# Kernel tuning notes

Measured on AMD Instinct MI355X. Metric: run time of the kernel, lower is better.

The kernel has to match this reference:

```python
import jax, jax.numpy as jnp
import numpy as np

EMBED = 1024
HEADS = 16
HEAD_DIM = EMBED // HEADS


def setup_inputs() -> dict:
    key = jax.random.key(0)
    ks = jax.random.split(key, 12)
    B, S, E = 2, 2048, EMBED
    scale = 1.0 / np.sqrt(E)
    inp = {
        "query": jax.random.normal(ks[0], (B, S, E), jnp.float32),
        "key": jax.random.normal(ks[1], (B, S, E), jnp.float32),
        "value": jax.random.normal(ks[2], (B, S, E), jnp.float32),
        "Wq": jax.random.normal(ks[3], (E, E), jnp.float32) * scale,
        "bq": jax.random.normal(ks[4], (E,), jnp.float32) * 0.01,
        "Wk": jax.random.normal(ks[5], (E, E), jnp.float32) * scale,
        "bk": jax.random.normal(ks[6], (E,), jnp.float32) * 0.01,
        "Wv": jax.random.normal(ks[7], (E, E), jnp.float32) * scale,
        "bv": jax.random.normal(ks[8], (E,), jnp.float32) * 0.01,
        "Wo": jax.random.normal(ks[9], (E, E), jnp.float32) * scale,
        "bo": jax.random.normal(ks[10], (E,), jnp.float32) * 0.01,
    }
    return inp


def reference(query, key, value, Wq, bq, Wk, bk, Wv, bv, Wo, bo):
    B, Sq, E = query.shape
    Sk = key.shape[1]
    H, D = HEADS, HEAD_DIM
    # QKV projections (torch Linear: x @ W.T + b)
    q = (query @ Wq.T + bq).reshape(B, Sq, H, D)
    k = (key @ Wk.T + bk).reshape(B, Sk, H, D)
    v = (value @ Wv.T + bv).reshape(B, Sk, H, D)
    # energy: [B, H, Sq, Sk]; note scale = 1/sqrt(embed_size), not head_dim
    energy = jnp.einsum("bqhd,bkhd->bhqk", q, k)
    scale = jnp.asarray(E, energy.dtype) ** 0.5
    attn = jax.nn.softmax(energy / scale, axis=-1)
    out = jnp.einsum("bhqk,bkhd->bqhd", attn, v).reshape(B, Sq, E)
    # fc_out (dropout is identity at eval)
    return out @ Wo.T + bo
```

## Files before the change

### kernel.cpp

```cpp
#include <hip/hip_runtime.h>
#include <hip/hip_bf16.h>

typedef __hip_bfloat16 bf16;
typedef short frag8 __attribute__((ext_vector_type(8)));
typedef _Float16 half4 __attribute__((ext_vector_type(4)));
typedef _Float16 half8 __attribute__((ext_vector_type(8)));
typedef __fp16 fp16x2 __attribute__((ext_vector_type(2)));
typedef float f32x4 __attribute__((ext_vector_type(4)));

typedef __attribute__((address_space(3))) void lds_void;
typedef __attribute__((address_space(1))) const void gbl_void;

__device__ __forceinline__ void gld16(const void* g, void* l) {
  __builtin_amdgcn_global_load_lds((gbl_void*)g, (lds_void*)l, 16, 0, 0);
}

__device__ __forceinline__ unsigned short f2bf(float f) {
  union { float f; unsigned u; } x; x.f = f;
  unsigned r = x.u + 0x7FFFu + ((x.u >> 16) & 1u);
  return (unsigned short)(r >> 16);
}

#define QSCALE 0.0450842200278f
#define MFIX 4.0f

struct CvtArgs {
  const float4* src[7];
  ushort4* dst[7];
  int n4[7];
};
__global__ __launch_bounds__(256) void cvt_all(CvtArgs a) {
  const int t = blockIdx.y;
  const int i = blockIdx.x * 256 + threadIdx.x;
  if (i >= a.n4[t]) return;
  float4 v = a.src[t][i];
  ushort4 o;
  o.x = f2bf(v.x); o.y = f2bf(v.y); o.z = f2bf(v.z); o.w = f2bf(v.w);
  a.dst[t][i] = o;
}

__device__ __forceinline__ void mfma32(f32x4 (&acc)[8][4], const frag8 (&a8)[8], const frag8 (&b4)[4]) {
  __builtin_amdgcn_s_setprio(1);
  #pragma unroll
  for (int i = 0; i < 8; ++i) {
    #pragma unroll
    for (int j = 0; j < 4; ++j)
      acc[i][j] = __builtin_amdgcn_mfma_f32_16x16x32_bf16(a8[i], b4[j], acc[i][j], 0, 0, 0);
  }
  __builtin_amdgcn_s_setprio(0);
}

__global__ __launch_bounds__(512, 2)
void gemm_qkv256(const bf16* __restrict__ A0, const bf16* __restrict__ A1, const bf16* __restrict__ A2,
                 const bf16* __restrict__ W0, const bf16* __restrict__ W1, const bf16* __restrict__ W2,
                 const float* __restrict__ b0, const float* __restrict__ b1, const float* __restrict__ b2,
                 void* __restrict__ o0, void* __restrict__ o1, void* __restrict__ o2) {
  __shared__ __align__(16) bf16 As[2][16384];
  __shared__ __align__(16) bf16 Bs[2][16384];
  const int tid = threadIdx.x;
  const int wave = tid >> 6, lane = tid & 63, quad = lane >> 4, l16 = lane & 15;
  const int wm = wave >> 2, wn = wave & 3;
  const int bn = blockIdx.x, bm = blockIdx.y, z = blockIdx.z;

  const bf16* A = A0; const bf16* W = W0; const float* bias = b0; void* out = o0;
  if (z == 1) { A = A1; W = W1; bias = b1; out = o1; }
  else if (z == 2) { A = A2; W = W2; bias = b2; out = o2; }

  const bf16* Ab = A + (size_t)bm * 256 * 1024;
  const bf16* Wb = W + (size_t)bn * 256 * 1024;
  const int c0_ = tid & 3, r0_ = tid >> 2;
  const int gcp = ((c0_ ^ ((r0_ >> 1) & 3)) << 3);
  const int rc2 = (quad ^ ((l16 >> 1) & 3)) << 3;

  auto stage = [&](const bf16* src, int kt, int kh, bf16* dst) {
    #pragma unroll
    for (int is = 0; is < 2; ++is) {
      const int r = r0_ + is * 128;
      gld16(src + (size_t)r * 1024 + kt * 64 + kh * 32 + gcp,
            (void*)(dst + (is * 512 + tid) * 8));
    }
  };
  auto ldsA8 = [&](const bf16* ah, frag8 (&a8)[8]) {
    #pragma unroll
    for (int i = 0; i < 8; ++i)
      a8[i] = *(const frag8*)&ah[(wm * 128 + i * 16 + l16) * 32 + rc2];
  };
  auto ldsB4 = [&](const bf16* bh, frag8 (&b4)[4]) {
    #pragma unroll
    for (int j = 0; j < 4; ++j)
      b4[j] = *(const frag8*)&bh[(wn * 64 + j * 16 + l16) * 32 + rc2];
  };

  f32x4 acc[8][4];
  #pragma unroll
  for (int i = 0; i < 8; ++i)
    #pragma unroll
    for (int j = 0; j < 4; ++j)
      acc[i][j] = (f32x4){0.f, 0.f, 0.f, 0.f};

  stage(Ab, 0, 0, &As[0][0]);
  stage(Wb, 0, 0, &Bs[0][0]);
  stage(Ab, 0, 1, &As[0][8192]);
  stage(Wb, 0, 1, &Bs[0][8192]);
  asm volatile("s_waitcnt vmcnt(0)" ::: "memory");
  __builtin_amdgcn_s_barrier();

  #pragma unroll 1
  for (int t = 0; t < 15; ++t) {
    const int buf = t & 1, nb = buf ^ 1;
    const bf16* a0 = &As[buf][0];    const bf16* a1 = &As[buf][8192];
    const bf16* b0 = &Bs[buf][0];    const bf16* b1 = &Bs[buf][8192];

    stage(Ab, t + 1, 0, &As[nb][0]);
    stage(Wb, t + 1, 0, &Bs[nb][0]);
    stage(Ab, t + 1, 1, &As[nb][8192]);
    stage(Wb, t + 1, 1, &Bs[nb][8192]);

    frag8 a8[8], b4[4];
    ldsA8(a0, a8); ldsB4(b0, b4);
    mfma32(acc, a8, b4);
    ldsA8(a1, a8); ldsB4(b1, b4);
    mfma32(acc, a8, b4);

    asm volatile("s_waitcnt vmcnt(0)" ::: "memory");
    __builtin_amdgcn_s_barrier();
  }

  {
    const bf16* a0 = &As[1][0];    const bf16* a1 = &As[1][8192];
    const bf16* b0 = &Bs[1][0];    const bf16* b1 = &Bs[1][8192];
    frag8 a8[8], b4[4];
    ldsA8(a0, a8); ldsB4(b0, b4);
    mfma32(acc, a8, b4);
    ldsA8(a1, a8); ldsB4(b1, b4);
    mfma32(acc, a8, b4);
  }

  #pragma unroll
  for (int j = 0; j < 4; ++j) {
    const int col = bn * 256 + wn * 64 + j * 16 + l16;
    const float bv = bias[col];
    #pragma unroll
    for (int i = 0; i < 8; ++i) {
      #pragma unroll
      for (int r = 0; r < 4; ++r) {
        const int row = bm * 256 + wm * 128 + i * 16 + quad * 4 + r;
        float v = acc[i][j][r] + bv;
        const int b = row >> 11, s = row & 2047;
        const int hh = col >> 6, d = col & 63;
        const size_t bh = (size_t)(b * 16 + hh);
        if (z == 0) {
          v *= QSCALE;
          ((bf16*)out)[(bh * 2048 + s) * 64 + d] = __float2bfloat16(v);
        } else if (z == 1) {
          const int g = s >> 6, l32 = s & 31, G32 = (s >> 5) & 1;
          const int q_ = (l32 >> 3) & 3, t_ = (l32 >> 2) & 1, i_ = l32 & 3;
          const int r64 = G32 * 32 + t_ * 16 + q_ * 4 + i_;
          const size_t addr = bh * 131072 + (size_t)g * 4096 + (size_t)r64 * 64
                            + (size_t)(((d >> 3) ^ (r64 & 7)) << 3) + (d & 7);
          ((bf16*)out)[addr] = __float2bfloat16(v);
        } else {
          const int g = s >> 6, k = s & 63;
          const size_t addr = bh * 131072 + (size_t)g * 4096 + (size_t)d * 64
                            + (size_t)(((k >> 3) ^ (d & 7)) << 3) + (k & 7);
          ((_Float16*)out)[addr] = (_Float16)v;
        }
      }
    }
  }
}

template<int MODE>
__global__ __launch_bounds__(256)
void gemm_bt(const bf16* __restrict__ A0, const bf16* __restrict__ A1, const bf16* __restrict__ A2,
             const bf16* __restrict__ W0, const bf16* __restrict__ W1, const bf16* __restrict__ W2,
             const float* __restrict__ b0, const float* __restrict__ b1, const float* __restrict__ b2,
             void* __restrict__ o0, void* __restrict__ o1, void* __restrict__ o2) {
  constexpr int NK = 1024;
  constexpr int BN = (MODE == 1) ? 128 : 64;
  __shared__ __align__(16) bf16 As[2][128 * 32];
  __shared__ __align__(16) bf16 Bs[2][BN * 32];
  const int tid = threadIdx.x;
  const int wave = tid >> 6, lane = tid & 63, quad = lane >> 4, l16 = lane & 15;
  const int wm = wave >> 1, wn = wave & 1;
  const int bn = blockIdx.x, bm = blockIdx.y;

  const bf16* A = A0; const bf16* W = W0; const float* bias = b0; void* out = o0;

  const bf16* Ab = A + (size_t)bm * 128 * NK;
  const bf16* Wb = W + (size_t)bn * BN * NK;
  const int c0_ = tid & 3, r0_ = tid >> 2;
  const int rc = (quad ^ (l16 & 3)) << 3;

  auto stageA = [&](int k0, int buf) {
    #pragma unroll
    for (int is = 0; is < 2; ++is) {
      const int c = tid + is * 256;
      const int r = r0_ + is * 64;
      const int gc = (c0_ ^ (r & 3)) << 3;
      gld16(Ab + (size_t)r * NK + k0 + gc, (void*)(&As[buf][(size_t)c * 8]));
    }
  };
  auto stageW = [&](int k0, int buf) {
    const int r = r0_;
    const int gc = (c0_ ^ (r & 3)) << 3;
    gld16(Wb + (size_t)r * NK + k0 + gc, (void*)(&Bs[buf][(size_t)tid * 8]));
  };

  f32x4 acc[4][2];
  #pragma unroll
  for (int i = 0; i < 4; ++i)
    #pragma unroll
    for (int j = 0; j < 2; ++j)
      acc[i][j] = (f32x4){0.f, 0.f, 0.f, 0.f};

  stageA(0, 0); stageW(0, 0);
  #pragma unroll 2
  for (int kt = 0; kt < 32; ++kt) {
    __syncthreads();
    if (kt < 31) { stageA((kt + 1) * 32, (kt + 1) & 1); stageW((kt + 1) * 32, (kt + 1) & 1); }
    const bf16* as_ = As[kt & 1];
    const bf16* bs_ = Bs[kt & 1];
    frag8 af[4], bfr[2];
    #pragma unroll
    for (int i = 0; i < 4; ++i)
      af[i] = *(const frag8*)&as_[(wm * 64 + i * 16 + l16) * 32 + rc];
    #pragma unroll
    for (int j = 0; j < 2; ++j)
      bfr[j] = *(const frag8*)&bs_[(wn * 32 + j * 16 + l16) * 32 + rc];
    #pragma unroll
    for (int i = 0; i < 4; ++i)
      #pragma unroll
      for (int j = 0; j < 2; ++j)
        acc[i][j] = __builtin_amdgcn_mfma_f32_16x16x32_bf16(af[i], bfr[j], acc[i][j], 0, 0, 0);
  }

  #pragma unroll
  for (int j = 0; j < 2; ++j) {
    const int col = bn * 64 + wn * 32 + j * 16 + l16;
    const float bv = bias[col];
    #pragma unroll
    for (int i = 0; i < 4; ++i) {
      #pragma unroll
      for (int r = 0; r < 4; ++r) {
        const int row = bm * 128 + wm * 64 + i * 16 + quad * 4 + r;
        ((float*)out)[(size_t)row * 1024 + col] = acc[i][j][r] + bv;
      }
    }
  }
}

__global__ __launch_bounds__(512, 2)
void flash_attn(const bf16* __restrict__ Q, const bf16* __restrict__ K,
                const _Float16* __restrict__ Vt, bf16* __restrict__ ctx) {
  __shared__ __align__(16) char smem[65536];
  bf16* Ks = (bf16*)smem;
  _Float16* Vs = (_Float16*)(smem + 32768);
  const int tid = threadIdx.x;
  const int wave = tid >> 6, lane = tid & 63, quad = lane >> 4, l16 = lane & 15;
  const int qg = wave & 3, kvg = wave >> 2;
  const int bh = blockIdx.x, b = bh >> 4, h = bh & 15;
  const int q0 = blockIdx.y * 256 + qg * 64;
  const bf16* Qb = Q + (size_t)bh * 131072;
  const bf16* Kb = K + (size_t)bh * 131072;
  const _Float16* Vb = Vt + (size_t)bh * 131072;

  frag8 qf[4][2];
  #pragma unroll
  for (int qt = 0; qt < 4; ++qt)
    #pragma unroll
    for (int ks = 0; ks < 2; ++ks)
      qf[qt][ks] = *(const frag8*)(Qb + (size_t)(q0 + qt * 16 + l16) * 64 + ks * 32 + quad * 8);

  f32x4 rsv[4];
  f32x4 o[4][4];
  #pragma unroll
  for (int qt = 0; qt < 4; ++qt) {
    rsv[qt] = (f32x4){0.f, 0.f, 0.f, 0.f};
    #pragma unroll
    for (int dt = 0; dt < 4; ++dt)
      o[qt][dt] = (f32x4){0.f, 0.f, 0.f, 0.f};
  }

  const int xk = l16 & 7;

  auto stage = [&](int kt, int buf) {
    #pragma unroll
    for (int s = 0; s < 2; ++s) {
      const int g = s * 16 + kt;
      gld16(Kb + (size_t)g * 4096 + (size_t)tid * 8, (void*)(Ks + (s * 2 + buf) * 4096 + tid * 8));
      gld16(Vb + (size_t)g * 4096 + (size_t)tid * 8, (void*)(Vs + (s * 2 + buf) * 4096 + tid * 8));
    }
  };

  stage(0, 0);
  #pragma unroll 2
  for (int kt = 0; kt < 16; ++kt) {
    __syncthreads();
    if (kt < 15) stage(kt + 1, (kt + 1) & 1);
    const bf16* ks_ = Ks + (kvg * 2 + (kt & 1)) * 4096;
    const _Float16* vs_ = Vs + (kvg * 2 + (kt & 1)) * 4096;

    f32x4 s[4][4];
    #pragma unroll
    for (int qt = 0; qt < 4; ++qt)
      #pragma unroll
      for (int jt = 0; jt < 4; ++jt)
        s[qt][jt] = (f32x4){-MFIX, -MFIX, -MFIX, -MFIX};
    #pragma unroll
    for (int ks = 0; ks < 2; ++ks) {
      frag8 kf[4];
      #pragma unroll
      for (int jt = 0; jt < 4; ++jt)
        kf[jt] = *(const frag8*)&ks_[(jt * 16 + l16) * 64 + (((ks * 4 + quad) ^ xk) << 3)];
      __builtin_amdgcn_s_setprio(1);
      #pragma unroll
      for (int qt = 0; qt < 4; ++qt)
        #pragma unroll
        for (int jt = 0; jt < 4; ++jt)
          s[qt][jt] = __builtin_amdgcn_mfma_f32_16x16x32_bf16(kf[jt], qf[qt][ks], s[qt][jt], 0, 0, 0);
      __builtin_amdgcn_s_setprio(0);
    }

    half8 pb[4][2];
    #pragma unroll
    for (int qt = 0; qt < 4; ++qt) {
      #pragma unroll
      for (int jt = 0; jt < 4; ++jt) {
        f32x4 p4;
        #pragma unroll
        for (int r = 0; r < 4; ++r)
          p4[r] = __builtin_amdgcn_exp2f(s[qt][jt][r]);
        rsv[qt] += p4;
        union { fp16x2 h2[2]; half4 h4; } u;
        u.h2[0] = __builtin_amdgcn_cvt_pkrtz(p4[0], p4[1]);
        u.h2[1] = __builtin_amdgcn_cvt_pkrtz(p4[2], p4[3]);
        const int jtp = jt >> 1, hi = (jt & 1) * 4;
        pb[qt][jtp][hi + 0] = u.h4[0];
        pb[qt][jtp][hi + 1] = u.h4[1];
        pb[qt][jtp][hi + 2] = u.h4[2];
        pb[qt][jtp][hi + 3] = u.h4[3];
      }
    }

    #pragma unroll
    for (int jtp = 0; jtp < 2; ++jtp) {
      half8 vf[4];
      #pragma unroll
      for (int dt = 0; dt < 4; ++dt)
        vf[dt] = *(const half8*)&vs_[(dt * 16 + l16) * 64 + (((jtp * 4 + quad) ^ xk) << 3)];
      __builtin_amdgcn_s_setprio(1);
      #pragma unroll
      for (int qt = 0; qt < 4; ++qt)
        #pragma unroll
        for (int dt = 0; dt < 4; ++dt)
          o[qt][dt] = __builtin_amdgcn_mfma_f32_16x16x32_f16(vf[dt], pb[qt][jtp], o[qt][dt], 0, 0, 0);
      __builtin_amdgcn_s_setprio(0);
    }
  }

  float4* mo = (float4*)smem;
  float*  ml = (float*)(smem + 32768);
  const int mbase = (qg * 64 + lane) * 8;
  #pragma unroll
  for (int r = 0; r < 2; ++r) {
    __syncthreads();
    if (kvg == 1) {
      #pragma unroll
      for (int qh = 0; qh < 2; ++qh) {
        const int qt = r * 2 + qh;
        #pragma unroll
        for (int dt = 0; dt < 4; ++dt) {
          const int i = qh * 4 + dt;
          mo[mbase + (i ^ (lane & 7))] = (float4){o[qt][dt][0], o[qt][dt][1], o[qt][dt][2], o[qt][dt][3]};
        }
        ml[(qg * 64 + lane) * 2 + qh] = rsv[qt][0] + rsv[qt][1] + rsv[qt][2] + rsv[qt][3];
      }
    }
    __syncthreads();
    if (kvg == 0) {
      #pragma unroll
      for (int qh = 0; qh < 2; ++qh) {
        const int qt = r * 2 + qh;
        float l = rsv[qt][0] + rsv[qt][1] + rsv[qt][2] + rsv[qt][3]
                + ml[(qg * 64 + lane) * 2 + qh];
        l += __shfl_xor(l, 16, 64);
        l += __shfl_xor(l, 32, 64);
        const float inv = __builtin_amdgcn_rcpf(l);
        const int q = q0 + qt * 16 + l16;
        #pragma unroll
        for (int dt = 0; dt < 4; ++dt) {
          const int i = qh * 4 + dt;
          const float4 po = mo[mbase + (i ^ (lane & 7))];
          ushort4 w;
          w.x = f2bf((o[qt][dt][0] + po.x) * inv);
          w.y = f2bf((o[qt][dt][1] + po.y) * inv);
          w.z = f2bf((o[qt][dt][2] + po.z) * inv);
          w.w = f2bf((o[qt][dt][3] + po.w) * inv);
          const int d = dt * 16 + quad * 4;
          *(uint2*)&ctx[((size_t)(b * 2048 + q)) * 1024 + h * 64 + d] = *(uint2*)&w;
        }
      }
    }
  }
}

extern "C" void kernel_launch(void* const* d_in, const int* in_sizes, int n_in,
                              void* d_out, int out_size, void* d_ws, size_t ws_size,
                              hipStream_t stream) {
  const float* q_in = (const float*)d_in[0];
  const float* k_in = (const float*)d_in[1];
  const float* v_in = (const float*)d_in[2];
  const float* Wq = (const float*)d_in[3];
  const float* bq = (const float*)d_in[4];
  const float* Wk = (const float*)d_in[5];
  const float* bk = (const float*)d_in[6];
  const float* Wv = (const float*)d_in[7];
  const float* bv = (const float*)d_in[8];
  const float* Wo = (const float*)d_in[9];
  const float* bo = (const float*)d_in[10];

  char* ws = (char*)d_ws;
  const size_t MB = 1024 * 1024;
  bf16* Xq  = (bf16*)(ws + 0 * MB);
  bf16* Xk  = (bf16*)(ws + 8 * MB);
  bf16* Xv  = (bf16*)(ws + 16 * MB);
  bf16* Wqb = (bf16*)(ws + 24 * MB);
  bf16* Wkb = (bf16*)(ws + 26 * MB);
  bf16* Wvb = (bf16*)(ws + 28 * MB);
  bf16* Wob = (bf16*)(ws + 30 * MB);
  bf16* Qw  = (bf16*)(ws + 32 * MB);
  bf16* Kw  = (bf16*)(ws + 40 * MB);
  _Float16* Vtw = (_Float16*)(ws + 48 * MB);
  bf16* Ctx = (bf16*)(ws + 56 * MB);

  {
    CvtArgs a;
    a.src[0] = (const float4*)q_in; a.dst[0] = (ushort4*)Xq;  a.n4[0] = 4194304 / 4;
    a.src[1] = (const float4*)k_in; a.dst[1] = (ushort4*)Xk;  a.n4[1] = 4194304 / 4;
    a.src[2] = (const float4*)v_in; a.dst[2] = (ushort4*)Xv;  a.n4[2] = 4194304 / 4;
    a.src[3] = (const float4*)Wq;   a.dst[3] = (ushort4*)Wqb; a.n4[3] = 1048576 / 4;
    a.src[4] = (const float4*)Wk;   a.dst[4] = (ushort4*)Wkb; a.n4[4] = 1048576 / 4;
    a.src[5] = (const float4*)Wv;   a.dst[5] = (ushort4*)Wvb; a.n4[5] = 1048576 / 4;
    a.src[6] = (const float4*)Wo;   a.dst[6] = (ushort4*)Wob; a.n4[6] = 1048576 / 4;
    cvt_all<<<dim3(4096, 7), 256, 0, stream>>>(a);
  }

  gemm_qkv256<<<dim3(4, 16, 3), 512, 0, stream>>>(Xq, Xk, Xv, Wqb, Wkb, Wvb,
                                                  bq, bk, bv, Qw, Kw, (bf16*)Vtw);
  flash_attn<<<dim3(32, 8), 512, 0, stream>>>(Qw, Kw, Vtw, Ctx);
  gemm_bt<0><<<dim3(16, 32), 256, 0, stream>>>(Ctx, nullptr, nullptr, Wob, nullptr, nullptr,
                                               bo, nullptr, nullptr, d_out, nullptr, nullptr);
}
```

Before: 236.7 us.

## Deepen QKV GEMM pipeline to four stages and stage V output through LDS

Replaces the double-buffered K loop (64-wide steps, full drain each iteration) with a 4-deep ring of 32-wide K slices. It uses partial vmcnt waits so three global-to-LDS loads stay in flight while MFMAs run. For the V projection, the fp16 transposed tile is first written into LDS in its swizzled layout and then copied out with 16-byte coalesced stores, replacing scattered 2-byte stores. The cost is more barriers per K element and reuse of the same 128 KB of LDS for the epilogue.

```diff
diff --git a/kernel.cpp b/kernel.cpp
--- a/kernel.cpp
+++ b/kernel.cpp
@@ -55,8 +55,9 @@
                  const bf16* __restrict__ W0, const bf16* __restrict__ W1, const bf16* __restrict__ W2,
                  const float* __restrict__ b0, const float* __restrict__ b1, const float* __restrict__ b2,
                  void* __restrict__ o0, void* __restrict__ o1, void* __restrict__ o2) {
-  __shared__ __align__(16) bf16 As[2][16384];
-  __shared__ __align__(16) bf16 Bs[2][16384];
+  __shared__ __align__(16) char smem[131072];
+  bf16* As = (bf16*)smem;
+  bf16* Bs = (bf16*)(smem + 65536);
   const int tid = threadIdx.x;
   const int wave = tid >> 6, lane = tid & 63, quad = lane >> 4, l16 = lane & 15;
   const int wm = wave >> 2, wn = wave & 3;
@@ -72,12 +73,18 @@
   const int gcp = ((c0_ ^ ((r0_ >> 1) & 3)) << 3);
   const int rc2 = (quad ^ ((l16 >> 1) & 3)) << 3;
 
-  auto stage = [&](const bf16* src, int kt, int kh, bf16* dst) {
+  auto stageA = [&](int kt, bf16* dst) {
     #pragma unroll
     for (int is = 0; is < 2; ++is) {
       const int r = r0_ + is * 128;
-      gld16(src + (size_t)r * 1024 + kt * 64 + kh * 32 + gcp,
-            (void*)(dst + (is * 512 + tid) * 8));
+      gld16(Ab + (size_t)r * 1024 + kt * 32 + gcp, (void*)(dst + (is * 512 + tid) * 8));
+    }
+  };
+  auto stageW = [&](int kt, bf16* dst) {
+    #pragma unroll
+    for (int is = 0; is < 2; ++is) {
+      const int r = r0_ + is * 128;
+      gld16(Wb + (size_t)r * 1024 + kt * 32 + gcp, (void*)(dst + (is * 512 + tid) * 8));
     }
   };
   auto ldsA8 = [&](const bf16* ah, frag8 (&a8)[8]) {
@@ -98,72 +105,113 @@
     for (int j = 0; j < 4; ++j)
       acc[i][j] = (f32x4){0.f, 0.f, 0.f, 0.f};
 
-  stage(Ab, 0, 0, &As[0][0]);
-  stage(Wb, 0, 0, &Bs[0][0]);
-  stage(Ab, 0, 1, &As[0][8192]);
-  stage(Wb, 0, 1, &Bs[0][8192]);
-  asm volatile("s_waitcnt vmcnt(0)" ::: "memory");
-  __builtin_amdgcn_s_barrier();
-
-  #pragma unroll 1
-  for (int t = 0; t < 15; ++t) {
-    const int buf = t & 1, nb = buf ^ 1;
-    const bf16* a0 = &As[buf][0];    const bf16* a1 = &As[buf][8192];
-    const bf16* b0 = &Bs[buf][0];    const bf16* b1 = &Bs[buf][8192];
-
-    stage(Ab, t + 1, 0, &As[nb][0]);
-    stage(Wb, t + 1, 0, &Bs[nb][0]);
-    stage(Ab, t + 1, 1, &As[nb][8192]);
-    stage(Wb, t + 1, 1, &Bs[nb][8192]);
-
+  stageA(0, As + 0 * 8192); stageW(0, Bs + 0 * 8192);
+  stageA(1, As + 1 * 8192); stageW(1, Bs + 1 * 8192);
+  stageA(2, As + 2 * 8192); stageW(2, Bs + 2 * 8192);
+
+  #pragma unroll 4
+  for (int t = 0; t < 28; ++t) {
+    asm volatile("s_waitcnt vmcnt(8)" ::: "memory");
+    __builtin_amdgcn_s_barrier();
+    const bf16* ab = As + (t & 3) * 8192;
+    const bf16* bb = Bs + (t & 3) * 8192;
     frag8 a8[8], b4[4];
-    ldsA8(a0, a8); ldsB4(b0, b4);
+    ldsA8(ab, a8); ldsB4(bb, b4);
+    stageA(t + 3, As + ((t + 3) & 3) * 8192);
+    stageW(t + 3, Bs + ((t + 3) & 3) * 8192);
+    asm volatile("s_waitcnt lgkmcnt(0)" ::: "memory");
     mfma32(acc, a8, b4);
-    ldsA8(a1, a8); ldsB4(b1, b4);
+  }
+  {
+    asm volatile("s_waitcnt vmcnt(8)" ::: "memory");
+    __builtin_amdgcn_s_barrier();
+    frag8 a8[8], b4[4];
+    ldsA8(As + 0 * 8192, a8); ldsB4(Bs + 0 * 8192, b4);
+    stageA(31, As + 3 * 8192);
+    stageW(31, Bs + 3 * 8192);
+    asm volatile("s_waitcnt lgkmcnt(0)" ::: "memory");
     mfma32(acc, a8, b4);
-
+  }
+  {
+    asm volatile("s_waitcnt vmcnt(8)" ::: "memory");
+    __builtin_amdgcn_s_barrier();
+    frag8 a8[8], b4[4];
+    ldsA8(As + 1 * 8192, a8); ldsB4(Bs + 1 * 8192, b4);
+    asm volatile("s_waitcnt lgkmcnt(0)" ::: "memory");
+    mfma32(acc, a8, b4);
+  }
+  {
+    asm volatile("s_waitcnt vmcnt(4)" ::: "memory");
+    __builtin_amdgcn_s_barrier();
+    frag8 a8[8], b4[4];
+    ldsA8(As + 2 * 8192, a8); ldsB4(Bs + 2 * 8192, b4);
+    asm volatile("s_waitcnt lgkmcnt(0)" ::: "memory");
+    mfma32(acc, a8, b4);
+  }
+  {
     asm volatile("s_waitcnt vmcnt(0)" ::: "memory");
     __builtin_amdgcn_s_barrier();
-  }
-
-  {
-    const bf16* a0 = &As[1][0];    const bf16* a1 = &As[1][8192];
-    const bf16* b0 = &Bs[1][0];    const bf16* b1 = &Bs[1][8192];
     frag8 a8[8], b4[4];
-    ldsA8(a0, a8); ldsB4(b0, b4);
+    ldsA8(As + 3 * 8192, a8); ldsB4(Bs + 3 * 8192, b4);
+    asm volatile("s_waitcnt lgkmcnt(0)" ::: "memory");
     mfma32(acc, a8, b4);
-    ldsA8(a1, a8); ldsB4(b1, b4);
-    mfma32(acc, a8, b4);
-  }
-
-  #pragma unroll
-  for (int j = 0; j < 4; ++j) {
-    const int col = bn * 256 + wn * 64 + j * 16 + l16;
-    const float bv = bias[col];
-    #pragma unroll
-    for (int i = 0; i < 8; ++i) {
-      #pragma unroll
-      for (int r = 0; r < 4; ++r) {
-        const int row = bm * 256 + wm * 128 + i * 16 + quad * 4 + r;
-        float v = acc[i][j][r] + bv;
-        const int b = row >> 11, s = row & 2047;
-        const int hh = col >> 6, d = col & 63;
-        const size_t bh = (size_t)(b * 16 + hh);
-        if (z == 0) {
-          v *= QSCALE;
-          ((bf16*)out)[(bh * 2048 + s) * 64 + d] = __float2bfloat16(v);
-        } else if (z == 1) {
-          const int g = s >> 6, l32 = s & 31, G32 = (s >> 5) & 1;
-          const int q_ = (l32 >> 3) & 3, t_ = (l32 >> 2) & 1, i_ = l32 & 3;
-          const int r64 = G32 * 32 + t_ * 16 + q_ * 4 + i_;
-          const size_t addr = bh * 131072 + (size_t)g * 4096 + (size_t)r64 * 64
-                            + (size_t)(((d >> 3) ^ (r64 & 7)) << 3) + (d & 7);
-          ((bf16*)out)[addr] = __float2bfloat16(v);
-        } else {
-          const int g = s >> 6, k = s & 63;
-          const size_t addr = bh * 131072 + (size_t)g * 4096 + (size_t)d * 64
-                            + (size_t)(((k >> 3) ^ (d & 7)) << 3) + (k & 7);
-          ((_Float16*)out)[addr] = (_Float16)v;
+  }
+
+  if (z == 2) {
+    _Float16* vlds = (_Float16*)smem;
+    __builtin_amdgcn_s_barrier();
+    #pragma unroll
+    for (int j = 0; j < 4; ++j) {
+      const int col = bn * 256 + wn * 64 + j * 16 + l16;
+      const float bv = bias[col];
+      const int d = j * 16 + l16;
+      #pragma unroll
+      for (int i = 0; i < 8; ++i) {
+        const int g = wm * 2 + (i >> 2);
+        const int kb = (i & 3) * 16 + quad * 4;
+        half4 h;
+        #pragma unroll
+        for (int r = 0; r < 4; ++r)
+          h[r] = (_Float16)(acc[i][j][r] + bv);
+        const int off = ((wn * 4 + g) << 12) + d * 64 + ((((kb >> 3) ^ (d & 7)) << 3)) + (kb & 7);
+        *(half4*)&vlds[off] = h;
+      }
+    }
+    __builtin_amdgcn_s_barrier();
+    const int b_ = bm >> 3;
+    #pragma unroll
+    for (int rd = 0; rd < 16; ++rd) {
+      const int l = rd * 4096 + tid * 8;
+      const int wnp = l >> 14, g = (l >> 12) & 3, off = l & 4095;
+      const size_t bhp = (size_t)(b_ * 16 + bn * 4 + wnp);
+      const size_t addr = bhp * 131072 + (size_t)((bm & 7) * 4 + g) * 4096 + (size_t)off;
+      *(uint4*)&((_Float16*)out)[addr] = *(const uint4*)&vlds[l];
+    }
+  } else {
+    #pragma unroll
+    for (int j = 0; j < 4; ++j) {
+      const int col = bn * 256 + wn * 64 + j * 16 + l16;
+      const float bv = bias[col];
+      #pragma unroll
+      for (int i = 0; i < 8; ++i) {
+        #pragma unroll
+        for (int r = 0; r < 4; ++r) {
+          const int row = bm * 256 + wm * 128 + i * 16 + quad * 4 + r;
+          float v = acc[i][j][r] + bv;
+          const int b = row >> 11, s = row & 2047;
+          const int hh = col >> 6, d = col & 63;
+          const size_t bh = (size_t)(b * 16 + hh);
+          if (z == 0) {
+            v *= QSCALE;
+            ((bf16*)out)[(bh * 2048 + s) * 64 + d] = __float2bfloat16(v);
+          } else {
+            const int g = s >> 6, l32 = s & 31, G32 = (s >> 5) & 1;
+            const int q_ = (l32 >> 3) & 3, t_ = (l32 >> 2) & 1, i_ = l32 & 3;
+            const int r64 = G32 * 32 + t_ * 16 + q_ * 4 + i_;
+            const size_t addr = bh * 131072 + (size_t)g * 4096 + (size_t)r64 * 64
+                              + (size_t)(((d >> 3) ^ (r64 & 7)) << 3) + (d & 7);
+            ((bf16*)out)[addr] = __float2bfloat16(v);
+          }
         }
       }
     }
```

New measurement: 212.9 us. 10.1% less time.
